# Optimization experiments

Hardware: AMD Instinct MI355X
Metric: run time of the kernel (lower is better)

## Reference

```python
import jax, jax.numpy as jnp
import numpy as np

B, H, W, C = 16, 64, 64, 256
NH = 8
WS = (8, 8)          # window size
SS = (4, 4)          # shift size (sum>0 -> shifted path active)
N = WS[0] * WS[1]    # tokens per window = 64
nWh, nWw = H // WS[0], W // WS[1]
nW = nWh * nWw       # 64 windows
HD = C // NH         # head dim
EPS = 1e-5


def instance_norm(x):
    # x: [B,H,W,C]; InstanceNorm2d normalizes per (sample, channel) over H,W (biased var, no affine)
    m = jnp.mean(x, axis=(1, 2), keepdims=True)
    v = jnp.var(x, axis=(1, 2), keepdims=True)
    return (x - m) * jax.lax.rsqrt(v + EPS)


def to_windows(x):
    # [B,H,W,C] -> [B*nW, N, C]
    x = x.reshape(B, nWh, WS[0], nWw, WS[1], C).transpose(0, 1, 3, 2, 4, 5)
    return x.reshape(B * nW, N, C)


def from_windows(x):
    # [B*nW, N, C] -> [B,H,W,C]
    x = x.reshape(B, nWh, nWw, WS[0], WS[1], C).transpose(0, 1, 3, 2, 4, 5)
    return x.reshape(B, H, W, C)


def build_attn_mask():
    # static shapes -> build with numpy at trace time
    img = np.zeros((H, W), np.float32)
    cnt = 0
    h_sl = ((0, H - WS[0]), (H - WS[0], H - SS[0]), (H - SS[0], H))
    w_sl = ((0, W - WS[1]), (W - WS[1], W - SS[1]), (W - SS[1], W))
    for h0, h1 in h_sl:
        for w0, w1 in w_sl:
            img[h0:h1, w0:w1] = cnt
            cnt += 1
    m = img.reshape(nWh, WS[0], nWw, WS[1]).transpose(0, 2, 1, 3).reshape(nW, N)
    d = m[:, None, :] - m[:, :, None]  # [nW, N, N]
    return jnp.asarray(np.where(d != 0, -100.0, 0.0).astype(np.float32))


ATTN_MASK = build_attn_mask()  # [nW, N, N]


def setup_inputs() -> dict:
    key = jax.random.key(0)
    ks = jax.random.split(key, 13)
    d = {}
    d["input_q"] = jax.random.normal(ks[0], (B, H, W, C), jnp.float32)
    d["input_k"] = jax.random.normal(ks[1], (B, H, W, C), jnp.float32)
    d["input_v_scale"] = jax.random.normal(ks[2], (B, H, W, C), jnp.float32)
    d["input_v_shift"] = jax.random.normal(ks[3], (B, H, W, C), jnp.float32)
    d["k_weight"] = jax.random.normal(ks[4], (C, C), jnp.float32) * 0.02
    d["k_bias"] = jax.random.normal(ks[5], (C,), jnp.float32) * 0.02
    d["v_weight_scale"] = jax.random.normal(ks[6], (C, C), jnp.float32) * 0.02
    d["v_bias_scale"] = jax.random.normal(ks[7], (C,), jnp.float32) * 0.02
    d["v_weight_shift"] = jax.random.normal(ks[8], (C, C), jnp.float32) * 0.02
    d["v_bias_shift"] = jax.random.normal(ks[9], (C,), jnp.float32) * 0.02
    d["proj_weight"] = jax.random.normal(ks[10], (C, C), jnp.float32) * 0.02
    d["proj_bias"] = jax.random.normal(ks[11], (C,), jnp.float32) * 0.02
    d["relative_position_bias"] = jax.random.normal(ks[12], (1, NH, N, N), jnp.float32) * 0.02
    return d


def _heads(x):
    # [B*nW, N, C] -> [B*nW, NH, N, HD]
    return x.reshape(B * nW, N, NH, HD).transpose(0, 2, 1, 3)


def _out_branch(attn, v, proj_weight, proj_bias):
    # attn: [B*nW, NH, N, N]; v: [B*nW, NH, N, HD]
    x = jnp.einsum('whnm,whmd->whnd', attn, v)
    x = x.transpose(0, 2, 1, 3).reshape(B * nW, N, C)
    x = x @ proj_weight.T + proj_bias
    x = from_windows(x)
    return jnp.roll(x, shift=(SS[0], SS[1]), axis=(1, 2))  # reverse cyclic shift


def reference(input_q, input_k, input_v_scale, input_v_shift,
              k_weight, k_bias, v_weight_scale, v_bias_scale,
              v_weight_shift, v_bias_shift, proj_weight, proj_bias,
              relative_position_bias):
    # instance norm on q (k is normed after its linear; use_q_proj=False)
    q_in = instance_norm(input_q)

    # cyclic shift (no padding: H,W divisible by window)
    sh = (-SS[0], -SS[1])
    q_in = jnp.roll(q_in, shift=sh, axis=(1, 2))
    k_in = jnp.roll(input_k, shift=sh, axis=(1, 2))
    vs_in = jnp.roll(input_v_scale, shift=sh, axis=(1, 2))
    vsh_in = jnp.roll(input_v_shift, shift=sh, axis=(1, 2))

    q = to_windows(q_in)                                   # no q projection
    k = to_windows(k_in) @ k_weight.T + k_bias
    v_scale = to_windows(vs_in) @ v_weight_scale.T + v_bias_scale
    v_shift = to_windows(vsh_in) @ v_weight_shift.T + v_bias_shift

    # key instance-norm AFTER linear: unpartition -> norm over full map -> repartition
    k = to_windows(instance_norm(from_windows(k)))

    q = _heads(q) * (HD ** -0.5)
    k = _heads(k)
    v_scale = _heads(v_scale)
    v_shift = _heads(v_shift)

    attn = jnp.einsum('whnd,whmd->whnm', q, k) + relative_position_bias  # [B*nW,NH,N,N]
    attn = attn.reshape(B, nW, NH, N, N) + ATTN_MASK[None, :, None]
    attn = jax.nn.softmax(attn, axis=-1).reshape(B * nW, NH, N, N)

    x_scale = _out_branch(attn, v_scale, proj_weight, proj_bias)
    x_shift = _out_branch(attn, v_shift, proj_weight, proj_bias)
    return (x_scale, x_shift)
```

## Files before the change

### kernel.cpp

```cpp
#include <hip/hip_runtime.h>


typedef unsigned short u16;
typedef unsigned int u32;
typedef __attribute__((ext_vector_type(8))) short bf16x8;
typedef __attribute__((ext_vector_type(4))) float f32x4;

__device__ __forceinline__ float b2f(u16 u) {
  return __uint_as_float(((u32)u) << 16);
}
__device__ __forceinline__ u16 f2b(float f) {
  return __builtin_bit_cast(u16, (__bf16)f);
}
__device__ __forceinline__ u32 pk2(float a, float b) {
  return (u32)f2b(a) | ((u32)f2b(b) << 16);
}

__global__ __launch_bounds__(256) void stats_f32(const float* __restrict__ src,
                                                 float* __restrict__ ps,
                                                 float* __restrict__ pq) {
  const int blk = blockIdx.x;
  const int b = blk >> 6;
  const int p0 = (blk & 63) << 6;
  const int c = threadIdx.x;
  const float* p = src + (((size_t)(b << 12) + p0) << 8) + c;
  float s = 0.f, sq = 0.f;
#pragma unroll 8
  for (int i = 0; i < 64; ++i) {
    float v = p[(size_t)i << 8];
    s += v;
    sq = fmaf(v, v, sq);
  }
  ps[(blk << 8) + c] = s;
  pq[(blk << 8) + c] = sq;
}

__global__ void finalize_stats(const float* __restrict__ ps,
                               const float* __restrict__ pq,
                               float* __restrict__ A, float* __restrict__ Bo,
                               float scale) {
  const int i = blockIdx.x * 256 + threadIdx.x;
  const int b = i >> 8, c = i & 255;
  const float* s0 = ps + ((size_t)(b << 6) << 8) + c;
  const float* q0 = pq + ((size_t)(b << 6) << 8) + c;
  float s = 0.f, sq = 0.f;
#pragma unroll 8
  for (int j = 0; j < 64; ++j) {
    s += s0[(size_t)j << 8];
    sq += q0[(size_t)j << 8];
  }
  float m = s * (1.f / 4096.f);
  float v = sq * (1.f / 4096.f) - m * m;
  float a = rsqrtf(v + 1e-5f) * scale;
  A[i] = a;
  Bo[i] = -m * a;
}

__global__ __launch_bounds__(256) void rpbm_prep(const float* __restrict__ rpb,
                                                 float* __restrict__ rpbm) {
  const int idx = blockIdx.x * 256 + threadIdx.x;
  const int t = idx & 63;
  const int lane = (idx >> 6) & 63;
  const int h = (idx >> 12) & 7;
  const int var = idx >> 15;
  const int cf = t >> 4, rf = (t >> 2) & 3, r = t & 3;
  const int n = ((lane >> 4) << 2) + r + (rf << 4);
  const int m = (lane & 15) + (cf << 4);
  const int vh = var >> 1, vw = var & 1;
  const int ln = (vh ? (1 + ((n >> 3) >= 4)) : 0) * 3 + (vw ? (1 + ((n & 7) >= 4)) : 0);
  const int lm = (vh ? (1 + ((m >> 3) >= 4)) : 0) * 3 + (vw ? (1 + ((m & 7) >= 4)) : 0);
  rpbm[idx] = rpb[(h << 12) + (n << 6) + m] + ((ln == lm) ? 0.f : -100.f);
}

__global__ __launch_bounds__(256) void pwf_prep(const float* __restrict__ pW,
                                                u16* __restrict__ pwf) {
  const int idx = blockIdx.x * 256 + threadIdx.x;
  const int u_ = idx & 15, g_ = (idx >> 4) & 3, ks_ = (idx >> 6) & 7,
            cf_ = idx >> 9;
  const int oc = (cf_ << 4) + u_, ic = (ks_ << 5) + (g_ << 3);
  const float* p = pW + (size_t)oc * 256 + ic;
  float4 v0 = *(const float4*)p;
  float4 v1 = *(const float4*)(p + 4);
  uint4 w;
  w.x = pk2(v0.x, v0.y); w.y = pk2(v0.z, v0.w);
  w.z = pk2(v1.x, v1.y); w.w = pk2(v1.z, v1.w);
  *(uint4*)(pwf + (size_t)idx * 8) = w;
}

template <int MODE, int STATS>
__global__ __launch_bounds__(512) void gemm_lin(const float* src,
                                                const float* W,
                                                const float* bias,
                                                u16* dst,
                                                const float* src2,
                                                const float* W2,
                                                const float* bias2,
                                                u16* dst2,
                                                float* __restrict__ kps,
                                                float* __restrict__ kpq) {
  if (MODE == 1 && blockIdx.y == 1) {
    src = src2; W = W2; bias = bias2; dst = dst2;
  }
  __shared__ u16 A_s[128][72];
  __shared__ u16 B_s[256][72];
  const int t = threadIdx.x;
  const int r0 = blockIdx.x << 7;

  const int srowA = t >> 2;
  const int kA0 = (t & 3) << 4;
  const int rg = r0 + srowA;
  const int bb = rg >> 12;
  const int rr = rg & 4095;
  const int wi = rr >> 6;
  const int nn = rr & 63;
  const int hs = ((wi >> 3) << 3) + (nn >> 3);
  const int wsq = ((wi & 7) << 3) + (nn & 7);
  const size_t abase =
      (((size_t)((bb << 6) | ((hs + 4) & 63)) << 6) | ((wsq + 4) & 63)) << 8;
  const int srowB = t >> 1;
  const int kB0 = (t & 1) << 5;
  const size_t wbase = (size_t)srowB << 8;

  const int wid = t >> 6, l = t & 63, u = l & 15, g = l >> 4;
  const int wr = wid >> 2, wc = wid & 3;
  const int win = (blockIdx.x << 1) | wr;

  f32x4 acc[4][4];
#pragma unroll
  for (int i = 0; i < 4; ++i)
#pragma unroll
    for (int j = 0; j < 4; ++j) acc[i][j] = {0.f, 0.f, 0.f, 0.f};

  for (int kk = 0; kk < 256; kk += 64) {
    __syncthreads();
    {
      const float* ap = src + abase + kk + kA0;
#pragma unroll
      for (int j = 0; j < 2; ++j) {
        float4 v0 = *(const float4*)(ap + (j << 3));
        float4 v1 = *(const float4*)(ap + (j << 3) + 4);
        uint4 w;
        w.x = pk2(v0.x, v0.y); w.y = pk2(v0.z, v0.w);
        w.z = pk2(v1.x, v1.y); w.w = pk2(v1.z, v1.w);
        *(uint4*)&A_s[srowA][kA0 + (j << 3)] = w;
      }
      const float* bp = W + wbase + kk + kB0;
#pragma unroll
      for (int j = 0; j < 4; ++j) {
        float4 v0 = *(const float4*)(bp + (j << 3));
        float4 v1 = *(const float4*)(bp + (j << 3) + 4);
        uint4 x;
        x.x = pk2(v0.x, v0.y); x.y = pk2(v0.z, v0.w);
        x.z = pk2(v1.x, v1.y); x.w = pk2(v1.z, v1.w);
        *(uint4*)&B_s[srowB][kB0 + (j << 3)] = x;
      }
    }
    __syncthreads();
#pragma unroll
    for (int ks = 0; ks < 2; ++ks) {
      bf16x8 a[4], bq[4];
#pragma unroll
      for (int rf = 0; rf < 4; ++rf)
        a[rf] = *(const bf16x8*)&A_s[(wr << 6) + (rf << 4) + u][(ks << 5) + (g << 3)];
#pragma unroll
      for (int cf = 0; cf < 4; ++cf)
        bq[cf] = *(const bf16x8*)&B_s[(wc << 6) + (cf << 4) + u][(ks << 5) + (g << 3)];
#pragma unroll
      for (int rf = 0; rf < 4; ++rf)
#pragma unroll
        for (int cf = 0; cf < 4; ++cf)
          acc[rf][cf] = __builtin_amdgcn_mfma_f32_16x16x32_bf16(a[rf], bq[cf],
                                                                acc[rf][cf], 0, 0, 0);
    }
  }

#pragma unroll
  for (int cf = 0; cf < 4; ++cf) {
    const int col = (wc << 6) + (cf << 4) + u;
    const float bv = bias[col];
    float s = 0.f, sq = 0.f;
#pragma unroll
    for (int rf = 0; rf < 4; ++rf) {
      if (MODE == 0) {
        const int hh = col >> 5;
        const int ga = (col >> 3) & 3;
        const int j = col & 7;
        const size_t base =
            ((size_t)((win << 3) | hh) << 11) + (rf << 9) + (ga << 7) + j;
#pragma unroll
        for (int r = 0; r < 4; ++r) {
          u16 hv = f2b(acc[rf][cf][r] + bv);
          dst[base + (((g << 2) + r) << 3)] = hv;
          if (STATS) {
            float rv = b2f(hv);
            s += rv;
            sq = fmaf(rv, rv, sq);
          }
        }
      } else {
        const int hh = (wc << 1) | (cf >> 1);
        const int df = cf & 1;
        const int ks = rf >> 1;
        const int ga = ((rf & 1) << 1) | (g >> 1);
        const size_t base = ((size_t)((win << 3) | hh) << 11) + (df << 10) +
                            (ks << 9) + (ga << 7) + (u << 3) + ((g & 1) << 2);
        u32 w0 = pk2(acc[rf][cf][0] + bv, acc[rf][cf][1] + bv);
        u32 w1 = pk2(acc[rf][cf][2] + bv, acc[rf][cf][3] + bv);
        *(uint2*)(dst + base) = make_uint2(w0, w1);
      }
    }
    if (MODE == 0 && STATS) {
      s += __shfl_xor(s, 16);
      s += __shfl_xor(s, 32);
      sq += __shfl_xor(sq, 16);
      sq += __shfl_xor(sq, 32);
      if (g == 0) {
        const int row = (blockIdx.x << 1) | wr;
        kps[(row << 8) + col] = s;
        kpq[(row << 8) + col] = sq;
      }
    }
  }
}

__global__ __launch_bounds__(512) void attn_mega(
    const float* __restrict__ qsrc, const float* __restrict__ qA_,
    const float* __restrict__ qB_, const u16* __restrict__ klin,
    const float* __restrict__ kA_, const float* __restrict__ kB_,
    const u16* __restrict__ vt, const float* __restrict__ rpbm,
    const u16* __restrict__ pwf, const float* __restrict__ pbias,
    float* __restrict__ outp) {
  __shared__ u16 P[8][64][72];
  __shared__ u16 Xl[64][264];
  const int tid = threadIdx.x;
  const int wid = tid >> 6;
  const int l = tid & 63;
  const int u = l & 15;
  const int g = l >> 4;
  const int win = blockIdx.x;
  const int h = wid;
  const int b = win >> 6;
  const int wIdx = win & 63;
  const int wh = wIdx >> 3, ww = wIdx & 7;
  const int var = ((wh == 7) ? 2 : 0) | ((ww == 7) ? 1 : 0);
  const int coff = (h << 5) + (g << 3);

  float qav[8], qbv[8], kav[8], kbv[8];
  {
    const int o = (b << 8) + coff;
    float4 a0 = *(const float4*)(qA_ + o), a1 = *(const float4*)(qA_ + o + 4);
    float4 b0 = *(const float4*)(qB_ + o), b1 = *(const float4*)(qB_ + o + 4);
    float4 c0v = *(const float4*)(kA_ + o), c1 = *(const float4*)(kA_ + o + 4);
    float4 d0v = *(const float4*)(kB_ + o), d1 = *(const float4*)(kB_ + o + 4);
    qav[0]=a0.x;qav[1]=a0.y;qav[2]=a0.z;qav[3]=a0.w;qav[4]=a1.x;qav[5]=a1.y;qav[6]=a1.z;qav[7]=a1.w;
    qbv[0]=b0.x;qbv[1]=b0.y;qbv[2]=b0.z;qbv[3]=b0.w;qbv[4]=b1.x;qbv[5]=b1.y;qbv[6]=b1.z;qbv[7]=b1.w;
    kav[0]=c0v.x;kav[1]=c0v.y;kav[2]=c0v.z;kav[3]=c0v.w;kav[4]=c1.x;kav[5]=c1.y;kav[6]=c1.z;kav[7]=c1.w;
    kbv[0]=d0v.x;kbv[1]=d0v.y;kbv[2]=d0v.z;kbv[3]=d0v.w;kbv[4]=d1.x;kbv[5]=d1.y;kbv[6]=d1.z;kbv[7]=d1.w;
  }

  bf16x8 qf[4];
#pragma unroll
  for (int rf = 0; rf < 4; ++rf) {
    const int n = (rf << 4) + u;
    const int nhs = (wh << 3) + (n >> 3);
    const int nws = (ww << 3) + (n & 7);
    const float* qp = qsrc +
        ((((size_t)((b << 6) | ((nhs + 4) & 63)) << 6) | ((nws + 4) & 63)) << 8) + coff;
    float4 v0 = *(const float4*)qp;
    float4 v1 = *(const float4*)(qp + 4);
    float qv[8] = {v0.x, v0.y, v0.z, v0.w, v1.x, v1.y, v1.z, v1.w};
#pragma unroll
    for (int j = 0; j < 8; ++j) qf[rf][j] = (short)f2b(fmaf(qv[j], qav[j], qbv[j]));
  }

  const u16* kp = klin + ((size_t)((win << 3) | h) << 11);
  bf16x8 kf[4];
#pragma unroll
  for (int cf = 0; cf < 4; ++cf) {
    union { uint4 v; u16 s[8]; } raw;
    raw.v = *(const uint4*)(kp + (cf << 9) + (g << 7) + (u << 3));
#pragma unroll
    for (int j = 0; j < 8; ++j)
      kf[cf][j] = (short)f2b(fmaf(b2f(raw.s[j]), kav[j], kbv[j]));
  }

  f32x4 s[4][4];
  const f32x4 z4 = {0.f, 0.f, 0.f, 0.f};
#pragma unroll
  for (int rf = 0; rf < 4; ++rf)
#pragma unroll
    for (int cf = 0; cf < 4; ++cf)
      s[rf][cf] = __builtin_amdgcn_mfma_f32_16x16x32_bf16(qf[rf], kf[cf], z4, 0, 0, 0);

  const float* rb = rpbm + ((((var << 3) + h) << 6) + l) * 64;
#pragma unroll
  for (int cf = 0; cf < 4; ++cf)
#pragma unroll
    for (int rf = 0; rf < 4; ++rf) {
      float4 bv = *(const float4*)(rb + (cf << 4) + (rf << 2));
      s[rf][cf][0] += bv.x; s[rf][cf][1] += bv.y;
      s[rf][cf][2] += bv.z; s[rf][cf][3] += bv.w;
    }

  f32x4 inv[4];
#pragma unroll
  for (int rf = 0; rf < 4; ++rf) {
#pragma unroll
    for (int r = 0; r < 4; ++r) {
      float m0 = fmaxf(fmaxf(s[rf][0][r], s[rf][1][r]),
                       fmaxf(s[rf][2][r], s[rf][3][r]));
      m0 = fmaxf(m0, __shfl_xor(m0, 1));
      m0 = fmaxf(m0, __shfl_xor(m0, 2));
      m0 = fmaxf(m0, __shfl_xor(m0, 4));
      m0 = fmaxf(m0, __shfl_xor(m0, 8));
      float t0 = 0.f;
#pragma unroll
      for (int cf = 0; cf < 4; ++cf) {
        s[rf][cf][r] = __expf(s[rf][cf][r] - m0);
        t0 += s[rf][cf][r];
      }
      t0 += __shfl_xor(t0, 1);
      t0 += __shfl_xor(t0, 2);
      t0 += __shfl_xor(t0, 4);
      t0 += __shfl_xor(t0, 8);
      inv[rf][r] = 1.f / t0;
    }
  }

#pragma unroll
  for (int rf = 0; rf < 4; ++rf)
#pragma unroll
    for (int r = 0; r < 4; ++r) {
      const int n = (rf << 4) + (g << 2) + r;
#pragma unroll
      for (int cf = 0; cf < 4; ++cf)
        P[wid][n][(cf << 4) + u] = f2b(s[rf][cf][r] * inv[rf][r]);
    }

#pragma unroll 1
  for (int br = 0; br < 2; ++br) {
    const u16* vb = vt + (size_t)br * 16777216 + ((size_t)((win << 3) | h) << 11);
    bf16x8 vf[2][2];
#pragma unroll
    for (int df = 0; df < 2; ++df)
#pragma unroll
      for (int ks = 0; ks < 2; ++ks)
        vf[df][ks] = *(const bf16x8*)(vb + (df << 10) + (ks << 9) + (g << 7) + (u << 3));
    f32x4 xt[2][4];
#pragma unroll
    for (int df = 0; df < 2; ++df)
#pragma unroll
      for (int cf = 0; cf < 4; ++cf) xt[df][cf] = z4;
#pragma unroll
    for (int cf = 0; cf < 4; ++cf)
#pragma unroll
      for (int ks = 0; ks < 2; ++ks) {
        bf16x8 pf = *(const bf16x8*)&P[wid][(cf << 4) + u][(ks << 5) + (g << 3)];
        xt[0][cf] = __builtin_amdgcn_mfma_f32_16x16x32_bf16(vf[0][ks], pf, xt[0][cf], 0, 0, 0);
        xt[1][cf] = __builtin_amdgcn_mfma_f32_16x16x32_bf16(vf[1][ks], pf, xt[1][cf], 0, 0, 0);
      }
#pragma unroll
    for (int df = 0; df < 2; ++df)
#pragma unroll
      for (int cf = 0; cf < 4; ++cf) {
        const int tok = (cf << 4) + u;
        const int ch = (h << 5) + (df << 4) + (g << 2);
        *(u32*)&Xl[tok][ch] = pk2(xt[df][cf][0], xt[df][cf][1]);
        *(u32*)&Xl[tok][ch + 2] = pk2(xt[df][cf][2], xt[df][cf][3]);
      }
    __syncthreads();

    f32x4 acc[4][2];
#pragma unroll
    for (int mf = 0; mf < 4; ++mf)
#pragma unroll
      for (int cfi = 0; cfi < 2; ++cfi) acc[mf][cfi] = z4;
#pragma unroll
    for (int ks = 0; ks < 8; ++ks) {
      bf16x8 a[4];
#pragma unroll
      for (int mf = 0; mf < 4; ++mf)
        a[mf] = *(const bf16x8*)&Xl[(mf << 4) + u][(ks << 5) + (g << 3)];
      bf16x8 bw[2];
#pragma unroll
      for (int cfi = 0; cfi < 2; ++cfi) {
        const int cf = (wid << 1) | cfi;
        bw[cfi] = *(const bf16x8*)(pwf +
            ((((((size_t)(cf << 3) | ks) << 2) | g) << 4 | u) << 3));
      }
#pragma unroll
      for (int mf = 0; mf < 4; ++mf)
#pragma unroll
        for (int cfi = 0; cfi < 2; ++cfi)
          acc[mf][cfi] = __builtin_amdgcn_mfma_f32_16x16x32_bf16(a[mf], bw[cfi],
                                                                 acc[mf][cfi], 0, 0, 0);
    }

    float* ob = outp + (size_t)br * 16777216;
#pragma unroll
    for (int cfi = 0; cfi < 2; ++cfi) {
      const int oc = (((wid << 1) | cfi) << 4) + u;
      const float bv = pbias[oc];
#pragma unroll
      for (int mf = 0; mf < 4; ++mf) {
#pragma unroll
        for (int r = 0; r < 4; ++r) {
          const int tok = (mf << 4) + (g << 2) + r;
          const int nhs = (wh << 3) + (tok >> 3);
          const int nws = (ww << 3) + (tok & 7);
          ob[((((size_t)((b << 6) | ((nhs + 4) & 63)) << 6) |
               ((nws + 4) & 63)) << 8) + oc] = acc[mf][cfi][r] + bv;
        }
      }
    }
    __syncthreads();
  }
}

extern "C" void kernel_launch(void* const* d_in, const int* in_sizes, int n_in,
                              void* d_out, int out_size, void* d_ws,
                              size_t ws_size, hipStream_t stream) {
  (void)in_sizes; (void)n_in; (void)out_size; (void)ws_size;
  const float* q   = (const float*)d_in[0];
  const float* k   = (const float*)d_in[1];
  const float* vs  = (const float*)d_in[2];
  const float* vsh = (const float*)d_in[3];
  const float* kW  = (const float*)d_in[4];
  const float* kb  = (const float*)d_in[5];
  const float* vWs = (const float*)d_in[6];
  const float* vbs = (const float*)d_in[7];
  const float* vWh = (const float*)d_in[8];
  const float* vbh = (const float*)d_in[9];
  const float* pW  = (const float*)d_in[10];
  const float* pb  = (const float*)d_in[11];
  const float* rpb = (const float*)d_in[12];
  float* out = (float*)d_out;

  float* f = (float*)d_ws;
  float* qps = f;
  float* qpq = f + 262144;
  float* kps = f + 524288;
  float* kpq = f + 786432;
  float* qA  = f + 1048576;
  float* qB  = f + 1052672;
  float* kA  = f + 1056768;
  float* kB  = f + 1060864;
  float* rpbm = f + 1064960;
  u16* klin = (u16*)(f + 1196032);
  u16* vt   = (u16*)(f + 9584640);
  u16* pwf  = (u16*)(f + 26361856);

  stats_f32<<<1024, 256, 0, stream>>>(q, qps, qpq);
  finalize_stats<<<16, 256, 0, stream>>>(qps, qpq, qA, qB,
                                         0.17677669529663687f);
  rpbm_prep<<<512, 256, 0, stream>>>(rpb, rpbm);
  pwf_prep<<<32, 256, 0, stream>>>(pW, pwf);

  gemm_lin<0, 1><<<512, 512, 0, stream>>>(k, kW, kb, klin,
                                          nullptr, nullptr, nullptr, nullptr,
                                          kps, kpq);
  finalize_stats<<<16, 256, 0, stream>>>(kps, kpq, kA, kB, 1.0f);

  gemm_lin<1, 0><<<dim3(512, 2), 512, 0, stream>>>(vs, vWs, vbs, vt,
                                                   vsh, vWh, vbh, vt + 16777216,
                                                   nullptr, nullptr);

  attn_mega<<<1024, 512, 0, stream>>>(q, qA, qB, klin, kA, kB, vt, rpbm,
                                      pwf, pb, out);
}
```

Measured before the change: 224.7 us.

## Merge K and V projection GEMMs into one launch; alias attention LDS buffers

The K projection and the two V projections now run in a single gemm_all launch with a 3-slice grid, selecting operands at runtime by blockIdx.y. This removes one kernel launch and lets the three GEMMs share the GPU concurrently. In attn_mega the P and Xl shared-memory arrays are placed in a union, with the P fragments loaded into registers and a barrier added before Xl overwrites them. This cuts LDS per block to raise occupancy (launch bounds now request 4 blocks), at the cost of more registers and an extra __syncthreads. The softmax normalisation is also folded into the scores before they are written to P.

```diff
diff --git a/kernel.cpp b/kernel.cpp
--- a/kernel.cpp
+++ b/kernel.cpp
@@ -87,20 +87,20 @@
   *(uint4*)(pwf + (size_t)idx * 8) = w;
 }
 
-template <int MODE, int STATS>
-__global__ __launch_bounds__(512) void gemm_lin(const float* src,
-                                                const float* W,
-                                                const float* bias,
-                                                u16* dst,
-                                                const float* src2,
-                                                const float* W2,
-                                                const float* bias2,
-                                                u16* dst2,
-                                                float* __restrict__ kps,
-                                                float* __restrict__ kpq) {
-  if (MODE == 1 && blockIdx.y == 1) {
-    src = src2; W = W2; bias = bias2; dst = dst2;
-  }
+__global__ __launch_bounds__(512) void gemm_all(
+    const float* __restrict__ ksrc, const float* __restrict__ kW,
+    const float* __restrict__ kbias, u16* __restrict__ klin,
+    const float* __restrict__ vs, const float* __restrict__ vWs,
+    const float* __restrict__ vbs, const float* __restrict__ vsh,
+    const float* __restrict__ vWh, const float* __restrict__ vbh,
+    u16* __restrict__ vt, float* __restrict__ kps, float* __restrict__ kpq) {
+  const int mode = (blockIdx.y == 0) ? 0 : 1;
+  const float *src, *W, *bias;
+  u16* dst;
+  if (blockIdx.y == 0) { src = ksrc; W = kW;  bias = kbias; dst = klin; }
+  else if (blockIdx.y == 1) { src = vs;  W = vWs; bias = vbs; dst = vt; }
+  else { src = vsh; W = vWh; bias = vbh; dst = vt + 16777216; }
+
   __shared__ u16 A_s[128][72];
   __shared__ u16 B_s[256][72];
   const int t = threadIdx.x;
@@ -181,7 +181,7 @@
     float s = 0.f, sq = 0.f;
 #pragma unroll
     for (int rf = 0; rf < 4; ++rf) {
-      if (MODE == 0) {
+      if (mode == 0) {
         const int hh = col >> 5;
         const int ga = (col >> 3) & 3;
         const int j = col & 7;
@@ -191,11 +191,9 @@
         for (int r = 0; r < 4; ++r) {
           u16 hv = f2b(acc[rf][cf][r] + bv);
           dst[base + (((g << 2) + r) << 3)] = hv;
-          if (STATS) {
-            float rv = b2f(hv);
-            s += rv;
-            sq = fmaf(rv, rv, sq);
-          }
+          float rv = b2f(hv);
+          s += rv;
+          sq = fmaf(rv, rv, sq);
         }
       } else {
         const int hh = (wc << 1) | (cf >> 1);
@@ -209,29 +207,32 @@
         *(uint2*)(dst + base) = make_uint2(w0, w1);
       }
     }
-    if (MODE == 0 && STATS) {
+    if (mode == 0) {
       s += __shfl_xor(s, 16);
       s += __shfl_xor(s, 32);
       sq += __shfl_xor(sq, 16);
       sq += __shfl_xor(sq, 32);
       if (g == 0) {
-        const int row = (blockIdx.x << 1) | wr;
-        kps[(row << 8) + col] = s;
-        kpq[(row << 8) + col] = sq;
-      }
-    }
-  }
-}
-
-__global__ __launch_bounds__(512) void attn_mega(
+        kps[(win << 8) + col] = s;
+        kpq[(win << 8) + col] = sq;
+      }
+    }
+  }
+}
+
+union AttnSh {
+  u16 P[8][64][72];
+  u16 Xl[64][264];
+};
+
+__global__ __launch_bounds__(512, 4) void attn_mega(
     const float* __restrict__ qsrc, const float* __restrict__ qA_,
     const float* __restrict__ qB_, const u16* __restrict__ klin,
     const float* __restrict__ kA_, const float* __restrict__ kB_,
     const u16* __restrict__ vt, const float* __restrict__ rpbm,
     const u16* __restrict__ pwf, const float* __restrict__ pbias,
     float* __restrict__ outp) {
-  __shared__ u16 P[8][64][72];
-  __shared__ u16 Xl[64][264];
+  __shared__ AttnSh sh;
   const int tid = threadIdx.x;
   const int wid = tid >> 6;
   const int l = tid & 63;
@@ -302,7 +303,6 @@
       s[rf][cf][2] += bv.z; s[rf][cf][3] += bv.w;
     }
 
-  f32x4 inv[4];
 #pragma unroll
   for (int rf = 0; rf < 4; ++rf) {
 #pragma unroll
@@ -323,7 +323,9 @@
       t0 += __shfl_xor(t0, 2);
       t0 += __shfl_xor(t0, 4);
       t0 += __shfl_xor(t0, 8);
-      inv[rf][r] = 1.f / t0;
+      const float inv = 1.f / t0;
+#pragma unroll
+      for (int cf = 0; cf < 4; ++cf) s[rf][cf][r] *= inv;
     }
   }
 
@@ -334,8 +336,16 @@
       const int n = (rf << 4) + (g << 2) + r;
 #pragma unroll
       for (int cf = 0; cf < 4; ++cf)
-        P[wid][n][(cf << 4) + u] = f2b(s[rf][cf][r] * inv[rf][r]);
-    }
+        sh.P[wid][n][(cf << 4) + u] = f2b(s[rf][cf][r]);
+    }
+
+  bf16x8 pf[4][2];
+#pragma unroll
+  for (int cf = 0; cf < 4; ++cf)
+#pragma unroll
+    for (int ks = 0; ks < 2; ++ks)
+      pf[cf][ks] = *(const bf16x8*)&sh.P[wid][(cf << 4) + u][(ks << 5) + (g << 3)];
+  __syncthreads();
 
 #pragma unroll 1
   for (int br = 0; br < 2; ++br) {
@@ -355,9 +365,8 @@
     for (int cf = 0; cf < 4; ++cf)
 #pragma unroll
       for (int ks = 0; ks < 2; ++ks) {
-        bf16x8 pf = *(const bf16x8*)&P[wid][(cf << 4) + u][(ks << 5) + (g << 3)];
-        xt[0][cf] = __builtin_amdgcn_mfma_f32_16x16x32_bf16(vf[0][ks], pf, xt[0][cf], 0, 0, 0);
-        xt[1][cf] = __builtin_amdgcn_mfma_f32_16x16x32_bf16(vf[1][ks], pf, xt[1][cf], 0, 0, 0);
+        xt[0][cf] = __builtin_amdgcn_mfma_f32_16x16x32_bf16(vf[0][ks], pf[cf][ks], xt[0][cf], 0, 0, 0);
+        xt[1][cf] = __builtin_amdgcn_mfma_f32_16x16x32_bf16(vf[1][ks], pf[cf][ks], xt[1][cf], 0, 0, 0);
       }
 #pragma unroll
     for (int df = 0; df < 2; ++df)
@@ -365,8 +374,8 @@
       for (int cf = 0; cf < 4; ++cf) {
         const int tok = (cf << 4) + u;
         const int ch = (h << 5) + (df << 4) + (g << 2);
-        *(u32*)&Xl[tok][ch] = pk2(xt[df][cf][0], xt[df][cf][1]);
-        *(u32*)&Xl[tok][ch + 2] = pk2(xt[df][cf][2], xt[df][cf][3]);
+        *(u32*)&sh.Xl[tok][ch] = pk2(xt[df][cf][0], xt[df][cf][1]);
+        *(u32*)&sh.Xl[tok][ch + 2] = pk2(xt[df][cf][2], xt[df][cf][3]);
       }
     __syncthreads();
 
@@ -380,7 +389,7 @@
       bf16x8 a[4];
 #pragma unroll
       for (int mf = 0; mf < 4; ++mf)
-        a[mf] = *(const bf16x8*)&Xl[(mf << 4) + u][(ks << 5) + (g << 3)];
+        a[mf] = *(const bf16x8*)&sh.Xl[(mf << 4) + u][(ks << 5) + (g << 3)];
       bf16x8 bw[2];
 #pragma unroll
       for (int cfi = 0; cfi < 2; ++cfi) {
@@ -456,14 +465,11 @@
   rpbm_prep<<<512, 256, 0, stream>>>(rpb, rpbm);
   pwf_prep<<<32, 256, 0, stream>>>(pW, pwf);
 
-  gemm_lin<0, 1><<<512, 512, 0, stream>>>(k, kW, kb, klin,
-                                          nullptr, nullptr, nullptr, nullptr,
-                                          kps, kpq);
+  gemm_all<<<dim3(512, 3), 512, 0, stream>>>(k, kW, kb, klin,
+                                             vs, vWs, vbs,
+                                             vsh, vWh, vbh, vt,
+                                             kps, kpq);
   finalize_stats<<<16, 256, 0, stream>>>(kps, kpq, kA, kB, 1.0f);
-
-  gemm_lin<1, 0><<<dim3(512, 2), 512, 0, stream>>>(vs, vWs, vbs, vt,
-                                                   vsh, vWh, vbh, vt + 16777216,
-                                                   nullptr, nullptr);
 
   attn_mega<<<1024, 512, 0, stream>>>(q, qA, qB, klin, kA, kB, vt, rpbm,
                                       pwf, pb, out);
```

After: 272.3 us. 1.21x slower.
